# Kernel tuning notes

Hardware: AMD Instinct MI355X
Metric: run time of the kernel (lower is better)

Reference implementation:

```python
import jax, jax.numpy as jnp
import numpy as np

B, N, C = 4, 4096, 256
H, D, K = 8, 32, 16  # heads, dim_head, knn


def setup_inputs() -> dict:
    key = jax.random.key(0)
    ks = jax.random.split(key, 7)
    s = 1.0 / np.sqrt(C)
    return {
        "x": jax.random.normal(ks[0], (B, N, C), dtype=jnp.float32),
        "Wq": jax.random.normal(ks[1], (C, H * D), dtype=jnp.float32) * s,
        "bq": jnp.zeros((H * D,), dtype=jnp.float32),
        "Wk": jax.random.normal(ks[2], (C, H * D), dtype=jnp.float32) * s,
        "bk": jnp.zeros((H * D,), dtype=jnp.float32),
        "Wv": jax.random.normal(ks[3], (C, H * D), dtype=jnp.float32) * s,
        "bv": jnp.zeros((H * D,), dtype=jnp.float32),
    }


def _knn_indices(x):
    # squared euclidean distances per batch: [B, N, N]
    sq = jnp.sum(x * x, axis=-1)
    d2 = sq[:, :, None] + sq[:, None, :] - 2.0 * jnp.einsum("bnc,bmc->bnm", x, x)
    # exclude self-loops (loop=False)
    eye = jnp.eye(x.shape[1], dtype=bool)
    d2 = jnp.where(eye[None], jnp.inf, d2)
    # k nearest neighbors (smallest distance)
    _, idx = jax.lax.top_k(-d2, K)  # [B, N, K]
    return idx


def reference(x, Wq, bq, Wk, bk, Wv, bv):
    idx = _knn_indices(x)  # [B, N, K] neighbor (source) node ids per target node
    # gather neighbor features: [B, N, K, C]
    xj = jax.vmap(lambda xb, ib: xb[ib])(x, idx)
    q = (x @ Wq + bq).reshape(B, N, H, D)           # target-node queries
    ke = (xj @ Wk + bk).reshape(B, N, K, H, D)      # per-edge keys
    ve = (xj @ Wv + bv).reshape(B, N, K, H, D)      # per-edge values
    scale = 1.0 / np.sqrt(D)
    scores = jnp.einsum("bnhd,bnkhd->bnkh", q, ke) * scale
    alpha = jax.nn.softmax(scores, axis=2)          # softmax over each node's K neighbors
    out = jnp.einsum("bnkh,bnkhd->bnhd", alpha, ve)
    return out.reshape(B, N, H * D)
```

## Files before the change

### kernel.cpp

```cpp
#include <hip/hip_runtime.h>
#include <cstdint>
#include <cstddef>

#define N_ 4096
#define C_ 256

typedef _Float16 h8 __attribute__((ext_vector_type(8)));
typedef _Float16 h4 __attribute__((ext_vector_type(4)));
typedef float f4 __attribute__((ext_vector_type(4)));

__device__ __forceinline__ void gl2lds16(const void* g, void* l) {
  __builtin_amdgcn_global_load_lds((const __attribute__((address_space(1))) void*)g,
                                   (__attribute__((address_space(3))) void*)l, 16, 0, 0);
}

__device__ __forceinline__ void ce_asc(double& a, double& b) {
  double mn = fmin(a, b), mx = fmax(a, b);
  a = mn; b = mx;
}

__device__ __forceinline__ void sort8_asc(double* c) {
#pragma unroll
  for (int k = 2; k <= 8; k <<= 1)
#pragma unroll
    for (int j = k >> 1; j > 0; j >>= 1)
#pragma unroll
      for (int i = 0; i < 8; i++) {
        int l = i ^ j;
        if (l > i) {
          bool up = ((i & k) == 0);
          double a = c[i], b = c[l];
          double mn = fmin(a, b), mx = fmax(a, b);
          c[i] = up ? mn : mx;
          c[l] = up ? mx : mn;
        }
      }
}

__device__ __forceinline__ void merge8_top16(double* karr, const double* c) {
#pragma unroll
  for (int i = 0; i < 8; i++)
    karr[8 + i] = fmin(karr[8 + i], c[7 - i]);
#pragma unroll
  for (int j = 8; j > 0; j >>= 1)
#pragma unroll
    for (int i = 0; i < 16; i++) {
      int l = i ^ j;
      if (l > i) ce_asc(karr[i], karr[l]);
    }
}

__device__ __forceinline__ void merge16d(double* a, const double* b) {
#pragma unroll
  for (int i = 0; i < 16; i++) a[i] = fmin(a[i], b[15 - i]);
#pragma unroll
  for (int j = 8; j > 0; j >>= 1)
#pragma unroll
    for (int i = 0; i < 16; i++) {
      int l = i ^ j;
      if (l > i) {
        double mn = fmin(a[i], a[l]), mx = fmax(a[i], a[l]);
        a[i] = mn; a[l] = mx;
      }
    }
}

__global__ __launch_bounds__(256) void k_prep(const float* __restrict__ x,
                                              float* __restrict__ sq,
                                              _Float16* __restrict__ xh,
                                              _Float16* __restrict__ xl) {
  int wave = threadIdx.x >> 6, lane = threadIdx.x & 63;
  int row = blockIdx.x * 4 + wave;
  size_t off = (size_t)row * C_ + lane * 4;
  float4 v = *(const float4*)(x + off);
  h4 hi; hi[0] = (_Float16)v.x; hi[1] = (_Float16)v.y;
         hi[2] = (_Float16)v.z; hi[3] = (_Float16)v.w;
  h4 lo; lo[0] = (_Float16)(v.x - (float)hi[0]); lo[1] = (_Float16)(v.y - (float)hi[1]);
         lo[2] = (_Float16)(v.z - (float)hi[2]); lo[3] = (_Float16)(v.w - (float)hi[3]);
  *(h4*)(xh + off) = hi;
  *(h4*)(xl + off) = lo;
  float s = v.x * v.x + v.y * v.y + v.z * v.z + v.w * v.w;
  s += __shfl_xor(s, 32); s += __shfl_xor(s, 16); s += __shfl_xor(s, 8);
  s += __shfl_xor(s, 4);  s += __shfl_xor(s, 2);  s += __shfl_xor(s, 1);
  if (lane == 0) sq[row] = s;
}

__global__ __launch_bounds__(256) void k_wsplit(const float* __restrict__ Wq,
                                                const float* __restrict__ Wk,
                                                const float* __restrict__ Wv,
                                                _Float16* __restrict__ wh,
                                                _Float16* __restrict__ wl) {
  int g = blockIdx.x * 256 + threadIdx.x;
  int m = g >> 16, e = g & 65535;
  int k = e >> 8, j = e & 255;
  const float* W = (m == 0) ? Wq : ((m == 1) ? Wk : Wv);
  float v = W[k * 256 + j];
  _Float16 hi = (_Float16)v;
  _Float16 lo = (_Float16)(v - (float)hi);
  wh[m * 65536 + j * 256 + k] = hi;
  wl[m * 65536 + j * 256 + k] = lo;
}

__global__ __launch_bounds__(256, 3) void k_proj(const _Float16* __restrict__ xh,
                                                 const _Float16* __restrict__ xl,
                                                 const _Float16* __restrict__ wh,
                                                 const _Float16* __restrict__ wl,
                                                 const float* __restrict__ bqp,
                                                 const float* __restrict__ bkp,
                                                 const float* __restrict__ bvp,
                                                 float* __restrict__ qf,
                                                 _Float16* __restrict__ kh,
                                                 _Float16* __restrict__ vh) {
  int tid = threadIdx.x;
  int bid = blockIdx.x;
  int m   = bid >> 8;
  int rb  = (bid >> 1) & 127;
  int cp  = bid & 1;
  int wave = tid >> 6, lane = tid & 63, quad = lane >> 4, l16 = lane & 15;
  const float* bb = (m == 0) ? bqp : ((m == 1) ? bkp : bvp);
  int row0 = rb * 128 + wave * 32;

  h8 Ah[2][8], Al[2][8];
#pragma unroll
  for (int rt = 0; rt < 2; rt++)
#pragma unroll
    for (int kc = 0; kc < 8; kc++) {
      size_t off = (size_t)(row0 + rt * 16 + l16) * C_ + kc * 32 + quad * 8;
      Ah[rt][kc] = *(const h8*)(xh + off);
      Al[rt][kc] = *(const h8*)(xl + off);
    }
  const _Float16* whm = wh + (size_t)m * 65536;
  const _Float16* wlm = wl + (size_t)m * 65536;

  f4 acc[2][8];
#pragma unroll
  for (int rt = 0; rt < 2; rt++)
#pragma unroll
    for (int ct = 0; ct < 8; ct++) acc[rt][ct] = f4{0.f, 0.f, 0.f, 0.f};
#pragma unroll
  for (int kc = 0; kc < 8; kc++) {
#pragma unroll
    for (int ct = 0; ct < 8; ct++) {
      int col = cp * 128 + ct * 16 + l16;
      h8 bh = *(const h8*)(whm + (size_t)col * 256 + kc * 32 + quad * 8);
      h8 bl = *(const h8*)(wlm + (size_t)col * 256 + kc * 32 + quad * 8);
#pragma unroll
      for (int rt = 0; rt < 2; rt++) {
        acc[rt][ct] = __builtin_amdgcn_mfma_f32_16x16x32_f16(Ah[rt][kc], bh, acc[rt][ct], 0, 0, 0);
        acc[rt][ct] = __builtin_amdgcn_mfma_f32_16x16x32_f16(Ah[rt][kc], bl, acc[rt][ct], 0, 0, 0);
        acc[rt][ct] = __builtin_amdgcn_mfma_f32_16x16x32_f16(Al[rt][kc], bh, acc[rt][ct], 0, 0, 0);
      }
    }
  }
  _Float16* d16 = (m == 1) ? kh : vh;
#pragma unroll
  for (int rt = 0; rt < 2; rt++)
#pragma unroll
    for (int ct = 0; ct < 8; ct++) {
      int col = cp * 128 + ct * 16 + l16;
      float bias = bb[col];
#pragma unroll
      for (int i = 0; i < 4; i++) {
        int r = row0 + rt * 16 + quad * 4 + i;
        float o = acc[rt][ct][i] + bias;
        if (m == 0) qf[(size_t)r * C_ + col] = o;
        else        d16[(size_t)r * C_ + col] = (_Float16)o;
      }
    }
}

__global__ __launch_bounds__(256, 2) void k_knn(const _Float16* __restrict__ xh,
                                                const _Float16* __restrict__ xl,
                                                const float* __restrict__ sq,
                                                double* __restrict__ pd) {
  __shared__ __align__(16) _Float16 Bh[16 * 528];
  __shared__ __align__(16) _Float16 Bl[16 * 528];
  __shared__ __align__(16) float sc[128 * 36];
  __shared__ float sqS[32];

  int tid = threadIdx.x;
  int wave = tid >> 6, lane = tid & 63, quad = lane >> 4, l16 = lane & 15;
  int bid = blockIdx.x;
  int s4 = bid & 3, tile = (bid >> 2) & 31, b = bid >> 7;
  int bN = b * N_, n0 = tile * 128, src0g = s4 * 1024;

  h8 Ah[2][8], Al[2][8];
  int tb = bN + n0 + wave * 32;
#pragma unroll
  for (int rt = 0; rt < 2; rt++)
#pragma unroll
    for (int kc = 0; kc < 8; kc++) {
      size_t off = (size_t)(tb + rt * 16 + l16) * C_ + kc * 32 + quad * 8;
      Ah[rt][kc] = *(const h8*)(xh + off);
      Al[rt][kc] = *(const h8*)(xl + off);
    }
  float sqT[2][4];
#pragma unroll
  for (int rt = 0; rt < 2; rt++)
#pragma unroll
    for (int i = 0; i < 4; i++)
      sqT[rt][i] = sq[tb + rt * 16 + quad * 4 + i];

  double karr[16];
#pragma unroll
  for (int p = 0; p < 16; p++) karr[p] = 1e300;
  int rowo = tid & 127, half = tid >> 7;

  {
    const _Float16* gh = xh + (size_t)(bN + src0g) * C_ + lane * 8;
    const _Float16* gl = xl + (size_t)(bN + src0g) * C_ + lane * 8;
#pragma unroll
    for (int k = 0; k < 4; k++) {
      int seg = wave * 4 + k;
      gl2lds16(gh + seg * 512, &Bh[seg * 528]);
      gl2lds16(gl + seg * 512, &Bl[seg * 528]);
    }
    if (tid < 32) sqS[tid] = sq[bN + src0g + tid];
  }

  int hb0 = ((l16 >> 1) * 528) + ((l16 & 1) * 256) + quad * 8;
  int hb1 = (((16 + l16) >> 1) * 528) + ((l16 & 1) * 256) + quad * 8;

#pragma unroll 1
  for (int ch = 0; ch < 32; ch++) {
    int src0 = src0g + ch * 32;
    __syncthreads();

    f4 acc[2][2];
#pragma unroll
    for (int rt = 0; rt < 2; rt++)
#pragma unroll
      for (int ct = 0; ct < 2; ct++) acc[rt][ct] = f4{0.f, 0.f, 0.f, 0.f};
#pragma unroll
    for (int kc = 0; kc < 8; kc++) {
      h8 bh0 = *(const h8*)(&Bh[hb0 + kc * 32]);
      h8 bh1 = *(const h8*)(&Bh[hb1 + kc * 32]);
      h8 bl0 = *(const h8*)(&Bl[hb0 + kc * 32]);
      h8 bl1 = *(const h8*)(&Bl[hb1 + kc * 32]);
#pragma unroll
      for (int rt = 0; rt < 2; rt++) {
        acc[rt][0] = __builtin_amdgcn_mfma_f32_16x16x32_f16(Ah[rt][kc], bh0, acc[rt][0], 0, 0, 0);
        acc[rt][0] = __builtin_amdgcn_mfma_f32_16x16x32_f16(Ah[rt][kc], bl0, acc[rt][0], 0, 0, 0);
        acc[rt][0] = __builtin_amdgcn_mfma_f32_16x16x32_f16(Al[rt][kc], bh0, acc[rt][0], 0, 0, 0);
        acc[rt][1] = __builtin_amdgcn_mfma_f32_16x16x32_f16(Ah[rt][kc], bh1, acc[rt][1], 0, 0, 0);
        acc[rt][1] = __builtin_amdgcn_mfma_f32_16x16x32_f16(Ah[rt][kc], bl1, acc[rt][1], 0, 0, 0);
        acc[rt][1] = __builtin_amdgcn_mfma_f32_16x16x32_f16(Al[rt][kc], bh1, acc[rt][1], 0, 0, 0);
      }
    }
    float sqSr[2] = {sqS[l16], sqS[16 + l16]};
#pragma unroll
    for (int rt = 0; rt < 2; rt++)
#pragma unroll
      for (int ct = 0; ct < 2; ct++) {
        int c = ct * 16 + l16;
#pragma unroll
        for (int i = 0; i < 4; i++) {
          int r = wave * 32 + rt * 16 + quad * 4 + i;
          float d2 = sqT[rt][i] + sqSr[ct] - 2.0f * acc[rt][ct][i];
          if (n0 + r == src0 + c) d2 = 1e38f;
          sc[r * 36 + c] = d2;
        }
      }
    __syncthreads();

    if (ch < 31) {
      int srcn = src0 + 32;
      const _Float16* gh = xh + (size_t)(bN + srcn) * C_ + lane * 8;
      const _Float16* gl = xl + (size_t)(bN + srcn) * C_ + lane * 8;
#pragma unroll
      for (int k = 0; k < 4; k++) {
        int seg = wave * 4 + k;
        gl2lds16(gh + seg * 512, &Bh[seg * 528]);
        gl2lds16(gl + seg * 512, &Bl[seg * 528]);
      }
      if (tid < 32) sqS[tid] = sq[bN + srcn + tid];
    }

#pragma unroll
    for (int bt = 0; bt < 2; bt++) {
      float dv[8];
#pragma unroll
      for (int k4 = 0; k4 < 2; k4++)
        *(float4*)&dv[k4 * 4] = *(const float4*)(&sc[rowo * 36 + half * 16 + bt * 8 + k4 * 4]);
      double c8[8];
#pragma unroll
      for (int j = 0; j < 8; j++) {
        double key = (double)dv[j];
        c8[j] = __longlong_as_double(__double_as_longlong(key) |
                                     (unsigned)(src0 + half * 16 + bt * 8 + j));
      }
      sort8_asc(c8);
      merge8_top16(karr, c8);
    }
  }

  __syncthreads();
  double* scd = (double*)sc;
  if (tid >= 128) {
#pragma unroll
    for (int p = 0; p < 16; p++) scd[(tid - 128) * 17 + p] = karr[p];
  }
  __syncthreads();
  if (tid < 128) {
#pragma unroll
    for (int i = 0; i < 16; i++)
      karr[i] = fmin(karr[i], scd[tid * 17 + (15 - i)]);
#pragma unroll
    for (int j = 8; j > 0; j >>= 1)
#pragma unroll
      for (int i = 0; i < 16; i++) {
        int l = i ^ j;
        if (l > i) ce_asc(karr[i], karr[l]);
      }
#pragma unroll
    for (int p = 0; p < 16; p++)
      pd[((size_t)bid * 128 + tid) * 16 + p] = karr[p];
  }
}

__global__ __launch_bounds__(64) void k_kmerge(const double* __restrict__ pd,
                                               int* __restrict__ idxo) {
  int g = blockIdx.x * 64 + threadIdx.x;
  int b = g >> 12, n = g & 4095;
  int tile = n >> 7, r = n & 127;
  size_t base = (size_t)(((b * 32 + tile) * 4) * 128 + r) * 16;

  double acc[16], other[16];
#pragma unroll
  for (int p = 0; p < 16; p++) acc[p] = pd[base + p];
#pragma unroll
  for (int s = 1; s < 4; s++) {
    size_t bs = base + (size_t)s * 128 * 16;
#pragma unroll
    for (int p = 0; p < 16; p++) other[p] = pd[bs + p];
    merge16d(acc, other);
  }
#pragma unroll
  for (int k = 0; k < 16; k++)
    idxo[(size_t)g * 16 + k] = (int)(__double_as_longlong(acc[k]) & 0xFFF);
}

__global__ __launch_bounds__(256) void k_attn(const float* __restrict__ qf,
                                              const _Float16* __restrict__ kh,
                                              const _Float16* __restrict__ vh,
                                              const int* __restrict__ idxv,
                                              float* __restrict__ out) {
  int wave = threadIdx.x >> 6, lane = threadIdx.x & 63;
  int g = blockIdx.x * 4 + wave;
  int bN = (g >> 12) << 12;
  float4 q4 = *(const float4*)(qf + (size_t)g * C_ + lane * 4);
  int my = idxv[(size_t)g * 16 + (lane & 15)];
  const float scale = 0.17677669529663687f;

  float s[16];
  h4 vv[16];
#pragma unroll
  for (int j = 0; j < 16; j++) {
    int nb = __shfl(my, j);
    size_t base = (size_t)(bN + nb) * C_ + lane * 4;
    h4 k4 = *(const h4*)(kh + base);
    vv[j] = *(const h4*)(vh + base);
    float p = (float)k4[0] * q4.x + (float)k4[1] * q4.y +
              (float)k4[2] * q4.z + (float)k4[3] * q4.w;
    p += __shfl_xor(p, 1); p += __shfl_xor(p, 2); p += __shfl_xor(p, 4);
    s[j] = p * scale;
  }
  float mx = s[0];
#pragma unroll
  for (int j = 1; j < 16; j++) mx = fmaxf(mx, s[j]);
  float den = 0.f;
#pragma unroll
  for (int j = 0; j < 16; j++) { s[j] = __expf(s[j] - mx); den += s[j]; }
  float inv = 1.0f / den;
  float4 o; o.x = 0.f; o.y = 0.f; o.z = 0.f; o.w = 0.f;
#pragma unroll
  for (int j = 0; j < 16; j++) {
    float w = s[j] * inv;
    o.x = fmaf(w, (float)vv[j][0], o.x); o.y = fmaf(w, (float)vv[j][1], o.y);
    o.z = fmaf(w, (float)vv[j][2], o.z); o.w = fmaf(w, (float)vv[j][3], o.w);
  }
  *(float4*)(out + (size_t)g * C_ + lane * 4) = o;
}

extern "C" void kernel_launch(void* const* d_in, const int* in_sizes, int n_in,
                              void* d_out, int out_size, void* d_ws, size_t ws_size,
                              hipStream_t stream) {
  const float* x  = (const float*)d_in[0];
  const float* Wq = (const float*)d_in[1];
  const float* bq = (const float*)d_in[2];
  const float* Wk = (const float*)d_in[3];
  const float* bk = (const float*)d_in[4];
  const float* Wv = (const float*)d_in[5];
  const float* bv = (const float*)d_in[6];
  float* out = (float*)d_out;

  char* ws = (char*)d_ws;
  float*     sqp  = (float*)(ws + 0);
  _Float16*  xh   = (_Float16*)(ws + 65536);
  _Float16*  xl   = (_Float16*)(ws + 8454144);
  float*     qf   = (float*)(ws + 16842752);
  _Float16*  khp  = (_Float16*)(ws + 33619968);
  _Float16*  vhp  = (_Float16*)(ws + 50397184);
  double*    pd   = (double*)(ws + 67174400);
  int*       idxb = (int*)  (ws + 75563008);
  _Float16*  whf  = (_Float16*)(ws + 76611584);
  _Float16*  wlf  = (_Float16*)(ws + 77004800);

  k_prep  <<<4096, 256, 0, stream>>>(x, sqp, xh, xl);
  k_wsplit<<<768,  256, 0, stream>>>(Wq, Wk, Wv, whf, wlf);
  k_proj  <<<768,  256, 0, stream>>>(xh, xl, whf, wlf, bq, bk, bv, qf, khp, vhp);
  k_knn   <<<512,  256, 0, stream>>>(xh, xl, sqp, pd);
  k_kmerge<<<256,  64,  0, stream>>>(pd, idxb);
  k_attn  <<<4096, 256, 0, stream>>>(qf, khp, vhp, idxb, out);
}
```

Baseline: 284.7 us.

## Double k_knn threads: one row tile per wave, four-way top-k split

Raises the k_knn block from 256 to 512 threads. Each wave now computes one 16-row tile instead of two, and each of the four thread groups per row does top-k over 8 candidates per chunk, followed by a three-step LDS tree merge of the partial top-16 lists. It also replaces the bitonic 8-element sort with a 19-comparator optimal network and interleaves the MFMA accumulator chains. The intent is more parallelism and latency hiding in the serial sort/merge phase, at the cost of more barriers and extra merge work at the end.

```diff
diff --git a/kernel.cpp b/kernel.cpp
--- a/kernel.cpp
+++ b/kernel.cpp
@@ -20,21 +20,12 @@
 }
 
 __device__ __forceinline__ void sort8_asc(double* c) {
-#pragma unroll
-  for (int k = 2; k <= 8; k <<= 1)
-#pragma unroll
-    for (int j = k >> 1; j > 0; j >>= 1)
-#pragma unroll
-      for (int i = 0; i < 8; i++) {
-        int l = i ^ j;
-        if (l > i) {
-          bool up = ((i & k) == 0);
-          double a = c[i], b = c[l];
-          double mn = fmin(a, b), mx = fmax(a, b);
-          c[i] = up ? mn : mx;
-          c[l] = up ? mx : mn;
-        }
-      }
+  ce_asc(c[0], c[1]); ce_asc(c[2], c[3]); ce_asc(c[4], c[5]); ce_asc(c[6], c[7]);
+  ce_asc(c[0], c[2]); ce_asc(c[1], c[3]); ce_asc(c[4], c[6]); ce_asc(c[5], c[7]);
+  ce_asc(c[1], c[2]); ce_asc(c[5], c[6]);
+  ce_asc(c[0], c[4]); ce_asc(c[1], c[5]); ce_asc(c[2], c[6]); ce_asc(c[3], c[7]);
+  ce_asc(c[2], c[4]); ce_asc(c[3], c[5]);
+  ce_asc(c[1], c[2]); ce_asc(c[3], c[4]); ce_asc(c[5], c[6]);
 }
 
 __device__ __forceinline__ void merge8_top16(double* karr, const double* c) {
@@ -169,7 +160,7 @@
     }
 }
 
-__global__ __launch_bounds__(256, 2) void k_knn(const _Float16* __restrict__ xh,
+__global__ __launch_bounds__(512, 3) void k_knn(const _Float16* __restrict__ xh,
                                                 const _Float16* __restrict__ xl,
                                                 const float* __restrict__ sq,
                                                 double* __restrict__ pd) {
@@ -184,34 +175,31 @@
   int s4 = bid & 3, tile = (bid >> 2) & 31, b = bid >> 7;
   int bN = b * N_, n0 = tile * 128, src0g = s4 * 1024;
 
-  h8 Ah[2][8], Al[2][8];
-  int tb = bN + n0 + wave * 32;
-#pragma unroll
-  for (int rt = 0; rt < 2; rt++)
-#pragma unroll
-    for (int kc = 0; kc < 8; kc++) {
-      size_t off = (size_t)(tb + rt * 16 + l16) * C_ + kc * 32 + quad * 8;
-      Ah[rt][kc] = *(const h8*)(xh + off);
-      Al[rt][kc] = *(const h8*)(xl + off);
-    }
-  float sqT[2][4];
-#pragma unroll
-  for (int rt = 0; rt < 2; rt++)
-#pragma unroll
-    for (int i = 0; i < 4; i++)
-      sqT[rt][i] = sq[tb + rt * 16 + quad * 4 + i];
+  h8 Ah[8], Al[8];
+  int tb = bN + n0 + wave * 16;
+#pragma unroll
+  for (int kc = 0; kc < 8; kc++) {
+    size_t off = (size_t)(tb + l16) * C_ + kc * 32 + quad * 8;
+    Ah[kc] = *(const h8*)(xh + off);
+    Al[kc] = *(const h8*)(xl + off);
+  }
+  float sqT[4];
+#pragma unroll
+  for (int i = 0; i < 4; i++)
+    sqT[i] = sq[tb + quad * 4 + i];
 
   double karr[16];
 #pragma unroll
   for (int p = 0; p < 16; p++) karr[p] = 1e300;
-  int rowo = tid & 127, half = tid >> 7;
+  int rown = tid & 127;
+  int part = tid >> 7;
 
   {
     const _Float16* gh = xh + (size_t)(bN + src0g) * C_ + lane * 8;
     const _Float16* gl = xl + (size_t)(bN + src0g) * C_ + lane * 8;
 #pragma unroll
-    for (int k = 0; k < 4; k++) {
-      int seg = wave * 4 + k;
+    for (int k = 0; k < 2; k++) {
+      int seg = wave * 2 + k;
       gl2lds16(gh + seg * 512, &Bh[seg * 528]);
       gl2lds16(gl + seg * 512, &Bl[seg * 528]);
     }
@@ -226,41 +214,34 @@
     int src0 = src0g + ch * 32;
     __syncthreads();
 
-    f4 acc[2][2];
-#pragma unroll
-    for (int rt = 0; rt < 2; rt++)
-#pragma unroll
-      for (int ct = 0; ct < 2; ct++) acc[rt][ct] = f4{0.f, 0.f, 0.f, 0.f};
+    f4 acc[2];
+    acc[0] = f4{0.f, 0.f, 0.f, 0.f};
+    acc[1] = f4{0.f, 0.f, 0.f, 0.f};
 #pragma unroll
     for (int kc = 0; kc < 8; kc++) {
       h8 bh0 = *(const h8*)(&Bh[hb0 + kc * 32]);
       h8 bh1 = *(const h8*)(&Bh[hb1 + kc * 32]);
       h8 bl0 = *(const h8*)(&Bl[hb0 + kc * 32]);
       h8 bl1 = *(const h8*)(&Bl[hb1 + kc * 32]);
-#pragma unroll
-      for (int rt = 0; rt < 2; rt++) {
-        acc[rt][0] = __builtin_amdgcn_mfma_f32_16x16x32_f16(Ah[rt][kc], bh0, acc[rt][0], 0, 0, 0);
-        acc[rt][0] = __builtin_amdgcn_mfma_f32_16x16x32_f16(Ah[rt][kc], bl0, acc[rt][0], 0, 0, 0);
-        acc[rt][0] = __builtin_amdgcn_mfma_f32_16x16x32_f16(Al[rt][kc], bh0, acc[rt][0], 0, 0, 0);
-        acc[rt][1] = __builtin_amdgcn_mfma_f32_16x16x32_f16(Ah[rt][kc], bh1, acc[rt][1], 0, 0, 0);
-        acc[rt][1] = __builtin_amdgcn_mfma_f32_16x16x32_f16(Ah[rt][kc], bl1, acc[rt][1], 0, 0, 0);
-        acc[rt][1] = __builtin_amdgcn_mfma_f32_16x16x32_f16(Al[rt][kc], bh1, acc[rt][1], 0, 0, 0);
+      acc[0] = __builtin_amdgcn_mfma_f32_16x16x32_f16(Ah[kc], bh0, acc[0], 0, 0, 0);
+      acc[1] = __builtin_amdgcn_mfma_f32_16x16x32_f16(Ah[kc], bh1, acc[1], 0, 0, 0);
+      acc[0] = __builtin_amdgcn_mfma_f32_16x16x32_f16(Ah[kc], bl0, acc[0], 0, 0, 0);
+      acc[1] = __builtin_amdgcn_mfma_f32_16x16x32_f16(Ah[kc], bl1, acc[1], 0, 0, 0);
+      acc[0] = __builtin_amdgcn_mfma_f32_16x16x32_f16(Al[kc], bh0, acc[0], 0, 0, 0);
+      acc[1] = __builtin_amdgcn_mfma_f32_16x16x32_f16(Al[kc], bh1, acc[1], 0, 0, 0);
+    }
+    float sqSr[2] = {sqS[l16], sqS[16 + l16]};
+#pragma unroll
+    for (int ct = 0; ct < 2; ct++) {
+      int c = ct * 16 + l16;
+#pragma unroll
+      for (int i = 0; i < 4; i++) {
+        int r = wave * 16 + quad * 4 + i;
+        float d2 = sqT[i] + sqSr[ct] - 2.0f * acc[ct][i];
+        if (n0 + r == src0 + c) d2 = 1e38f;
+        sc[r * 36 + c] = d2;
       }
     }
-    float sqSr[2] = {sqS[l16], sqS[16 + l16]};
-#pragma unroll
-    for (int rt = 0; rt < 2; rt++)
-#pragma unroll
-      for (int ct = 0; ct < 2; ct++) {
-        int c = ct * 16 + l16;
-#pragma unroll
-        for (int i = 0; i < 4; i++) {
-          int r = wave * 32 + rt * 16 + quad * 4 + i;
-          float d2 = sqT[rt][i] + sqSr[ct] - 2.0f * acc[rt][ct][i];
-          if (n0 + r == src0 + c) d2 = 1e38f;
-          sc[r * 36 + c] = d2;
-        }
-      }
     __syncthreads();
 
     if (ch < 31) {
@@ -268,53 +249,68 @@
       const _Float16* gh = xh + (size_t)(bN + srcn) * C_ + lane * 8;
       const _Float16* gl = xl + (size_t)(bN + srcn) * C_ + lane * 8;
 #pragma unroll
-      for (int k = 0; k < 4; k++) {
-        int seg = wave * 4 + k;
+      for (int k = 0; k < 2; k++) {
+        int seg = wave * 2 + k;
         gl2lds16(gh + seg * 512, &Bh[seg * 528]);
         gl2lds16(gl + seg * 512, &Bl[seg * 528]);
       }
       if (tid < 32) sqS[tid] = sq[bN + srcn + tid];
     }
 
-#pragma unroll
-    for (int bt = 0; bt < 2; bt++) {
-      float dv[8];
-#pragma unroll
-      for (int k4 = 0; k4 < 2; k4++)
-        *(float4*)&dv[k4 * 4] = *(const float4*)(&sc[rowo * 36 + half * 16 + bt * 8 + k4 * 4]);
-      double c8[8];
-#pragma unroll
-      for (int j = 0; j < 8; j++) {
-        double key = (double)dv[j];
-        c8[j] = __longlong_as_double(__double_as_longlong(key) |
-                                     (unsigned)(src0 + half * 16 + bt * 8 + j));
-      }
-      sort8_asc(c8);
-      merge8_top16(karr, c8);
-    }
-  }
-
-  __syncthreads();
-  double* scd = (double*)sc;
-  if (tid >= 128) {
-#pragma unroll
-    for (int p = 0; p < 16; p++) scd[(tid - 128) * 17 + p] = karr[p];
-  }
-  __syncthreads();
-  if (tid < 128) {
-#pragma unroll
-    for (int i = 0; i < 16; i++)
-      karr[i] = fmin(karr[i], scd[tid * 17 + (15 - i)]);
-#pragma unroll
-    for (int j = 8; j > 0; j >>= 1)
-#pragma unroll
-      for (int i = 0; i < 16; i++) {
-        int l = i ^ j;
-        if (l > i) ce_asc(karr[i], karr[l]);
-      }
+    float dv[8];
+#pragma unroll
+    for (int k4 = 0; k4 < 2; k4++)
+      *(float4*)&dv[k4 * 4] = *(const float4*)(&sc[rown * 36 + part * 8 + k4 * 4]);
+    double c8[8];
+#pragma unroll
+    for (int j = 0; j < 8; j++) {
+      double key = (double)dv[j];
+      c8[j] = __longlong_as_double(__double_as_longlong(key) |
+                                   (unsigned)(src0 + part * 8 + j));
+    }
+    sort8_asc(c8);
+    merge8_top16(karr, c8);
+  }
+
+  __syncthreads();
+  double* ex = (double*)sc;
+  if (part == 3) {
+#pragma unroll
+    for (int p = 0; p < 16; p++) ex[rown * 17 + p] = karr[p];
+  }
+  __syncthreads();
+  if (part == 2) {
+    double other[16];
+#pragma unroll
+    for (int p = 0; p < 16; p++) other[p] = ex[rown * 17 + p];
+    merge16d(karr, other);
+  }
+  __syncthreads();
+  if (part == 1) {
+#pragma unroll
+    for (int p = 0; p < 16; p++) ex[rown * 17 + p] = karr[p];
+  }
+  __syncthreads();
+  if (part == 0) {
+    double other[16];
+#pragma unroll
+    for (int p = 0; p < 16; p++) other[p] = ex[rown * 17 + p];
+    merge16d(karr, other);
+  }
+  __syncthreads();
+  if (part == 2) {
+#pragma unroll
+    for (int p = 0; p < 16; p++) ex[rown * 17 + p] = karr[p];
+  }
+  __syncthreads();
+  if (part == 0) {
+    double other[16];
+#pragma unroll
+    for (int p = 0; p < 16; p++) other[p] = ex[rown * 17 + p];
+    merge16d(karr, other);
 #pragma unroll
     for (int p = 0; p < 16; p++)
-      pd[((size_t)bid * 128 + tid) * 16 + p] = karr[p];
+      pd[((size_t)bid * 128 + rown) * 16 + p] = karr[p];
   }
 }
 
@@ -409,7 +405,7 @@
   k_prep  <<<4096, 256, 0, stream>>>(x, sqp, xh, xl);
   k_wsplit<<<768,  256, 0, stream>>>(Wq, Wk, Wv, whf, wlf);
   k_proj  <<<768,  256, 0, stream>>>(xh, xl, whf, wlf, bq, bk, bv, qf, khp, vhp);
-  k_knn   <<<512,  256, 0, stream>>>(xh, xl, sqp, pd);
+  k_knn   <<<512,  512, 0, stream>>>(xh, xl, sqp, pd);
   k_kmerge<<<256,  64,  0, stream>>>(pd, idxb);
   k_attn  <<<4096, 256, 0, stream>>>(qf, khp, vhp, idxb, out);
 }
```

After: 306.5 us. +7.7%, slower.

## Fuse prep kernels and fold top-k partial merge into attention via wave shuffles

Applied to the files above, without the earlier changes.

Merges the x-split and weight-split kernels into a single launch, and removes the standalone k-merge kernel. The attention kernel now reads the four partial top-16 lists directly and merges them with a cross-lane bitonic merge built from shuffles. The bitonic 8-sort is also replaced with a hand-written 19-comparator network. Two launches and the index buffer round trip go away, at the cost of extra shuffle work and redundant partial-list reads in every attention wave.

```diff
diff --git a/kernel.cpp b/kernel.cpp
--- a/kernel.cpp
+++ b/kernel.cpp
@@ -20,21 +20,12 @@
 }
 
 __device__ __forceinline__ void sort8_asc(double* c) {
-#pragma unroll
-  for (int k = 2; k <= 8; k <<= 1)
-#pragma unroll
-    for (int j = k >> 1; j > 0; j >>= 1)
-#pragma unroll
-      for (int i = 0; i < 8; i++) {
-        int l = i ^ j;
-        if (l > i) {
-          bool up = ((i & k) == 0);
-          double a = c[i], b = c[l];
-          double mn = fmin(a, b), mx = fmax(a, b);
-          c[i] = up ? mn : mx;
-          c[l] = up ? mx : mn;
-        }
-      }
+  ce_asc(c[0], c[1]); ce_asc(c[2], c[3]); ce_asc(c[4], c[5]); ce_asc(c[6], c[7]);
+  ce_asc(c[0], c[2]); ce_asc(c[1], c[3]); ce_asc(c[4], c[6]); ce_asc(c[5], c[7]);
+  ce_asc(c[1], c[2]); ce_asc(c[5], c[6]);
+  ce_asc(c[0], c[4]); ce_asc(c[1], c[5]); ce_asc(c[2], c[6]); ce_asc(c[3], c[7]);
+  ce_asc(c[2], c[4]); ce_asc(c[3], c[5]);
+  ce_asc(c[1], c[2]); ce_asc(c[3], c[4]); ce_asc(c[5], c[6]);
 }
 
 __device__ __forceinline__ void merge8_top16(double* karr, const double* c) {
@@ -50,55 +41,42 @@
     }
 }
 
-__device__ __forceinline__ void merge16d(double* a, const double* b) {
-#pragma unroll
-  for (int i = 0; i < 16; i++) a[i] = fmin(a[i], b[15 - i]);
-#pragma unroll
-  for (int j = 8; j > 0; j >>= 1)
-#pragma unroll
-    for (int i = 0; i < 16; i++) {
-      int l = i ^ j;
-      if (l > i) {
-        double mn = fmin(a[i], a[l]), mx = fmax(a[i], a[l]);
-        a[i] = mn; a[l] = mx;
-      }
-    }
-}
-
-__global__ __launch_bounds__(256) void k_prep(const float* __restrict__ x,
-                                              float* __restrict__ sq,
-                                              _Float16* __restrict__ xh,
-                                              _Float16* __restrict__ xl) {
-  int wave = threadIdx.x >> 6, lane = threadIdx.x & 63;
-  int row = blockIdx.x * 4 + wave;
-  size_t off = (size_t)row * C_ + lane * 4;
-  float4 v = *(const float4*)(x + off);
-  h4 hi; hi[0] = (_Float16)v.x; hi[1] = (_Float16)v.y;
-         hi[2] = (_Float16)v.z; hi[3] = (_Float16)v.w;
-  h4 lo; lo[0] = (_Float16)(v.x - (float)hi[0]); lo[1] = (_Float16)(v.y - (float)hi[1]);
-         lo[2] = (_Float16)(v.z - (float)hi[2]); lo[3] = (_Float16)(v.w - (float)hi[3]);
-  *(h4*)(xh + off) = hi;
-  *(h4*)(xl + off) = lo;
-  float s = v.x * v.x + v.y * v.y + v.z * v.z + v.w * v.w;
-  s += __shfl_xor(s, 32); s += __shfl_xor(s, 16); s += __shfl_xor(s, 8);
-  s += __shfl_xor(s, 4);  s += __shfl_xor(s, 2);  s += __shfl_xor(s, 1);
-  if (lane == 0) sq[row] = s;
-}
-
-__global__ __launch_bounds__(256) void k_wsplit(const float* __restrict__ Wq,
-                                                const float* __restrict__ Wk,
-                                                const float* __restrict__ Wv,
-                                                _Float16* __restrict__ wh,
-                                                _Float16* __restrict__ wl) {
-  int g = blockIdx.x * 256 + threadIdx.x;
-  int m = g >> 16, e = g & 65535;
-  int k = e >> 8, j = e & 255;
-  const float* W = (m == 0) ? Wq : ((m == 1) ? Wk : Wv);
-  float v = W[k * 256 + j];
-  _Float16 hi = (_Float16)v;
-  _Float16 lo = (_Float16)(v - (float)hi);
-  wh[m * 65536 + j * 256 + k] = hi;
-  wl[m * 65536 + j * 256 + k] = lo;
+__global__ __launch_bounds__(256) void k_pre(const float* __restrict__ x,
+                                             float* __restrict__ sq,
+                                             _Float16* __restrict__ xh,
+                                             _Float16* __restrict__ xl,
+                                             const float* __restrict__ Wq,
+                                             const float* __restrict__ Wk,
+                                             const float* __restrict__ Wv,
+                                             _Float16* __restrict__ wh,
+                                             _Float16* __restrict__ wl) {
+  int bid = blockIdx.x;
+  if (bid < 4096) {
+    int wave = threadIdx.x >> 6, lane = threadIdx.x & 63;
+    int row = bid * 4 + wave;
+    size_t off = (size_t)row * C_ + lane * 4;
+    float4 v = *(const float4*)(x + off);
+    h4 hi; hi[0] = (_Float16)v.x; hi[1] = (_Float16)v.y;
+           hi[2] = (_Float16)v.z; hi[3] = (_Float16)v.w;
+    h4 lo; lo[0] = (_Float16)(v.x - (float)hi[0]); lo[1] = (_Float16)(v.y - (float)hi[1]);
+           lo[2] = (_Float16)(v.z - (float)hi[2]); lo[3] = (_Float16)(v.w - (float)hi[3]);
+    *(h4*)(xh + off) = hi;
+    *(h4*)(xl + off) = lo;
+    float s = v.x * v.x + v.y * v.y + v.z * v.z + v.w * v.w;
+    s += __shfl_xor(s, 32); s += __shfl_xor(s, 16); s += __shfl_xor(s, 8);
+    s += __shfl_xor(s, 4);  s += __shfl_xor(s, 2);  s += __shfl_xor(s, 1);
+    if (lane == 0) sq[row] = s;
+  } else {
+    int g = (bid - 4096) * 256 + threadIdx.x;
+    int m = g >> 16, e = g & 65535;
+    int k = e >> 8, j = e & 255;
+    const float* W = (m == 0) ? Wq : ((m == 1) ? Wk : Wv);
+    float v = W[k * 256 + j];
+    _Float16 hi = (_Float16)v;
+    _Float16 lo = (_Float16)(v - (float)hi);
+    wh[m * 65536 + j * 256 + k] = hi;
+    wl[m * 65536 + j * 256 + k] = lo;
+  }
 }
 
 __global__ __launch_bounds__(256, 3) void k_proj(const _Float16* __restrict__ xh,
@@ -318,38 +296,34 @@
   }
 }
 
-__global__ __launch_bounds__(64) void k_kmerge(const double* __restrict__ pd,
-                                               int* __restrict__ idxo) {
-  int g = blockIdx.x * 64 + threadIdx.x;
-  int b = g >> 12, n = g & 4095;
-  int tile = n >> 7, r = n & 127;
-  size_t base = (size_t)(((b * 32 + tile) * 4) * 128 + r) * 16;
-
-  double acc[16], other[16];
-#pragma unroll
-  for (int p = 0; p < 16; p++) acc[p] = pd[base + p];
-#pragma unroll
-  for (int s = 1; s < 4; s++) {
-    size_t bs = base + (size_t)s * 128 * 16;
-#pragma unroll
-    for (int p = 0; p < 16; p++) other[p] = pd[bs + p];
-    merge16d(acc, other);
-  }
-#pragma unroll
-  for (int k = 0; k < 16; k++)
-    idxo[(size_t)g * 16 + k] = (int)(__double_as_longlong(acc[k]) & 0xFFF);
-}
-
 __global__ __launch_bounds__(256) void k_attn(const float* __restrict__ qf,
                                               const _Float16* __restrict__ kh,
                                               const _Float16* __restrict__ vh,
-                                              const int* __restrict__ idxv,
+                                              const double* __restrict__ pd,
                                               float* __restrict__ out) {
   int wave = threadIdx.x >> 6, lane = threadIdx.x & 63;
   int g = blockIdx.x * 4 + wave;
   int bN = (g >> 12) << 12;
+  int el = lane & 15;
+
+  int b = g >> 12, n = g & 4095;
+  int tile = n >> 7, r = n & 127;
+  size_t pbase = (size_t)(((b * 32 + tile) * 4) * 128 + r) * 16;
+  double a = pd[pbase + el];
+#pragma unroll
+  for (int s = 1; s < 4; s++) {
+    double bb = pd[pbase + (size_t)s * 128 * 16 + el];
+    double br = __shfl(bb, (lane & ~15) | (15 - el));
+    a = fmin(a, br);
+#pragma unroll
+    for (int j = 8; j > 0; j >>= 1) {
+      double o = __shfl(a, lane ^ j);
+      a = (el & j) ? fmax(a, o) : fmin(a, o);
+    }
+  }
+  int my = (int)(__double_as_longlong(a) & 0xFFF);
+
   float4 q4 = *(const float4*)(qf + (size_t)g * C_ + lane * 4);
-  int my = idxv[(size_t)g * 16 + (lane & 15)];
   const float scale = 0.17677669529663687f;
 
   float s[16];
@@ -402,14 +376,11 @@
   _Float16*  khp  = (_Float16*)(ws + 33619968);
   _Float16*  vhp  = (_Float16*)(ws + 50397184);
   double*    pd   = (double*)(ws + 67174400);
-  int*       idxb = (int*)  (ws + 75563008);
   _Float16*  whf  = (_Float16*)(ws + 76611584);
   _Float16*  wlf  = (_Float16*)(ws + 77004800);
 
-  k_prep  <<<4096, 256, 0, stream>>>(x, sqp, xh, xl);
-  k_wsplit<<<768,  256, 0, stream>>>(Wq, Wk, Wv, whf, wlf);
+  k_pre   <<<4864, 256, 0, stream>>>(x, sqp, xh, xl, Wq, Wk, Wv, whf, wlf);
   k_proj  <<<768,  256, 0, stream>>>(xh, xl, whf, wlf, bq, bk, bv, qf, khp, vhp);
   k_knn   <<<512,  256, 0, stream>>>(xh, xl, sqp, pd);
-  k_kmerge<<<256,  64,  0, stream>>>(pd, idxb);
-  k_attn  <<<4096, 256, 0, stream>>>(qf, khp, vhp, idxb, out);
-}
+  k_attn  <<<4096, 256, 0, stream>>>(qf, khp, vhp, pd, out);
+}
```

Measured after the change: 284.9 us (median of 2 runs). No clear change (+0.1%).
